# Kernel optimization log

Measured on AMD Instinct MI355X. Metric: run time of the kernel, lower is better.

## Reference

```python
import jax, jax.numpy as jnp
import numpy as np

HEADS = 20
HEAD_DIM = 64  # 1280 // 20
NUM_STYLE_TOKENS = 4
FU_SCALE = 0.5
STYLE_SCALE = 1.0
SCALE = np.float32(1.0 / np.sqrt(HEAD_DIM))


def setup_inputs() -> dict:
    key = jax.random.key(0)
    ks = jax.random.split(key, 9)
    B, S, D_MODEL, D_CROSS, T = 4, 4096, 1280, 768, 77
    sd_m = np.float32(1.0 / np.sqrt(D_MODEL))
    sd_c = np.float32(1.0 / np.sqrt(D_CROSS))
    return {
        "hidden_states": jax.random.normal(ks[0], (B, S, D_MODEL), jnp.float32),
        "encoder_hidden_states": jax.random.normal(ks[1], (B, T + NUM_STYLE_TOKENS, D_CROSS), jnp.float32),
        "Wq": jax.random.normal(ks[2], (D_MODEL, D_MODEL), jnp.float32) * sd_m,
        "Wk": jax.random.normal(ks[3], (D_CROSS, D_MODEL), jnp.float32) * sd_c,
        "Wv": jax.random.normal(ks[4], (D_CROSS, D_MODEL), jnp.float32) * sd_c,
        "Wk_ip": jax.random.normal(ks[5], (D_CROSS, D_MODEL), jnp.float32) * sd_c,
        "Wv_ip": jax.random.normal(ks[6], (D_CROSS, D_MODEL), jnp.float32) * sd_c,
        "Wo": jax.random.normal(ks[7], (D_MODEL, D_MODEL), jnp.float32) * sd_m,
        "bo": jnp.zeros((D_MODEL,), jnp.float32),
    }


def _split_heads(x, B):
    # [B, L, H*D] -> [B, H, L, D]
    return x.reshape(B, -1, HEADS, HEAD_DIM).transpose(0, 2, 1, 3)


def _attn_blend(q, k, v):
    # Manual QK^T softmax with cross-batch prob blending (fuAttn / fuIPAttn).
    probs = jax.nn.softmax(jnp.einsum('bhsd,bhtd->bhst', q, k) * SCALE, axis=-1)
    probs = probs.at[1].set(FU_SCALE * probs[1] + (1.0 - FU_SCALE) * probs[0])
    probs = probs.at[3].set(FU_SCALE * probs[3] + (1.0 - FU_SCALE) * probs[2])
    return jnp.einsum('bhst,bhtd->bhsd', probs, v)


def reference(hidden_states, encoder_hidden_states, Wq, Wk, Wv, Wk_ip, Wv_ip, Wo, bo):
    B, S, _ = hidden_states.shape
    end_pos = encoder_hidden_states.shape[1] - NUM_STYLE_TOKENS
    text = encoder_hidden_states[:, :end_pos, :]       # [B, 77, Dc]
    ip_style = encoder_hidden_states[:, end_pos:, :]   # [B, 4, Dc]

    q = _split_heads(hidden_states @ Wq, B)   # [B,H,S,D]
    k = _split_heads(text @ Wk, B)            # [B,H,77,D]
    v = _split_heads(text @ Wv, B)

    hid = _attn_blend(q, k, v).transpose(0, 2, 1, 3).reshape(B, S, -1)
    raw = hid

    ip_k = _split_heads(ip_style @ Wk_ip, B)  # [B,H,4,D]
    ip_v = _split_heads(ip_style @ Wv_ip, B)
    ip_hid = _attn_blend(q, ip_k, ip_v).transpose(0, 2, 1, 3).reshape(B, S, -1)

    hid = hid + STYLE_SCALE * ip_hid
    # batch rows 0 and 2 keep the raw (text-only) attention output
    hid = hid.at[0].set(raw[0]).at[2].set(raw[2])

    return hid @ Wo + bo
```

## Files before the change

### kernel.cpp

```cpp
#include <hip/hip_runtime.h>
#include <hip/hip_bf16.h>

typedef _Float16 half8 __attribute__((ext_vector_type(8)));
typedef _Float16 half4 __attribute__((ext_vector_type(4)));
typedef float floatx4 __attribute__((ext_vector_type(4)));

#define HEADS_ 20
#define B_    4
#define S_    4096
#define DM    1280
#define DC    768
#define TTOK  77
#define NST   4
#define EROWS 81
#define MROWS 324
#define NT_K  20

__device__ inline void gload_lds16(const void* g, void* l) {
  __builtin_amdgcn_global_load_lds((const __attribute__((address_space(1))) void*)g,
                                   (__attribute__((address_space(3))) void*)l, 16, 0, 0);
}

__global__ __launch_bounds__(256) void cast_f16(const float* __restrict__ in,
                                                _Float16* __restrict__ out, long n) {
  long i = ((long)blockIdx.x * 256 + threadIdx.x) * 8L;
  long stride = (long)gridDim.x * 256 * 8;
  for (; i < n; i += stride) {
    float4 a = *(const float4*)(in + i);
    float4 b = *(const float4*)(in + i + 4);
    half8 h;
    h[0] = (_Float16)a.x; h[1] = (_Float16)a.y; h[2] = (_Float16)a.z; h[3] = (_Float16)a.w;
    h[4] = (_Float16)b.x; h[5] = (_Float16)b.y; h[6] = (_Float16)b.z; h[7] = (_Float16)b.w;
    *(half8*)(out + i) = h;
  }
}

struct TParams { const float* in[6]; _Float16* out[6]; int R[6]; };

__global__ __launch_bounds__(256) void transpose_cast6(TParams p) {
  const int z = blockIdx.z;
  const int R = p.R[z];
  const int r0 = blockIdx.y * 32, c0 = blockIdx.x * 32;
  if (r0 >= R) return;
  const float* __restrict__ in = p.in[z];
  _Float16* __restrict__ out = p.out[z];
  __shared__ float t[32][33];
  int tx = threadIdx.x & 31, ty = threadIdx.x >> 5;
  #pragma unroll
  for (int j = 0; j < 32; j += 8)
    t[ty + j][tx] = in[(size_t)(r0 + ty + j) * DM + c0 + tx];
  __syncthreads();
  #pragma unroll
  for (int j = 0; j < 32; j += 8)
    out[(size_t)(c0 + ty + j) * R + r0 + tx] = (_Float16)t[tx][ty + j];
}

struct Ptrs4 { const _Float16* B[4]; _Float16* C[4]; };

__global__ __launch_bounds__(256) void gemm_kv(const _Float16* __restrict__ A,
                                               Ptrs4 p4, int M, int K, int N) {
  const int tid = threadIdx.x, lane = tid & 63, w = tid >> 6;
  const _Float16* Bp = p4.B[blockIdx.z];
  _Float16* Ch = p4.C[blockIdx.z];
  const int bm = blockIdx.x, bn = blockIdx.y;

  __shared__ _Float16 As[128 * 32];
  __shared__ _Float16 Bs[128 * 32];

  const int wr = (w >> 1) * 64, wc = (w & 1) * 64;
  const int arow = wr + (lane & 15), brow = wc + (lane & 15);
  const int koff = (lane >> 4) * 8;
  floatx4 acc[4][4] = {};

  const int nk = K >> 5;
  for (int kt = 0; kt < nk; ++kt) {
    #pragma unroll
    for (int c = 0; c < 2; ++c) {
      int l16 = w * 64 + lane + c * 256;
      int row = l16 >> 2, kc = (l16 & 3) << 3;
      int gr = bm * 128 + row; if (gr > M - 1) gr = M - 1;
      gload_lds16(A + (size_t)gr * K + kt * 32 + kc, &As[(w + c * 4) * 512]);
      int grb = bn * 128 + row;
      gload_lds16(Bp + (size_t)grb * K + kt * 32 + kc, &Bs[(w + c * 4) * 512]);
    }
    __syncthreads();
    half8 af[4], bf[4];
    #pragma unroll
    for (int m = 0; m < 4; m++) af[m] = *(const half8*)&As[(arow + m * 16) * 32 + koff];
    #pragma unroll
    for (int n = 0; n < 4; n++) bf[n] = *(const half8*)&Bs[(brow + n * 16) * 32 + koff];
    #pragma unroll
    for (int m = 0; m < 4; m++)
      #pragma unroll
      for (int n = 0; n < 4; n++)
        acc[m][n] = __builtin_amdgcn_mfma_f32_16x16x32_f16(af[m], bf[n], acc[m][n], 0, 0, 0);
    __syncthreads();
  }

  const int r0 = (lane >> 4) * 4, c0 = lane & 15;
  #pragma unroll
  for (int m = 0; m < 4; m++) {
    #pragma unroll
    for (int r = 0; r < 4; r++) {
      int grow = bm * 128 + wr + m * 16 + r0 + r;
      if (grow >= M) continue;
      size_t base = (size_t)grow * N + bn * 128 + wc + c0;
      #pragma unroll
      for (int n = 0; n < 4; n++) Ch[base + n * 16] = (_Float16)acc[m][n][r];
    }
  }
}

template<int OMODE>
__global__ __launch_bounds__(512, 2)
void gemm8(const _Float16* __restrict__ A,
           const _Float16* __restrict__ B,
           void* __restrict__ Cout,
           const float* __restrict__ bias) {
  __shared__ _Float16 lds[57344];
  _Float16* const A0 = lds;
  _Float16* const A1 = lds + 8192;
  _Float16* const B0 = lds + 16384;
  _Float16* const B1 = lds + 36864;

  const int tid = threadIdx.x, lane = tid & 63, w = tid >> 6;
  const int swz = (blockIdx.x & 7) * 64 + (blockIdx.x >> 3);
  const int bm = swz & 127, bn = swz >> 7;

  const int wr = w >> 2, wc = w & 3;
  const int ql = lane & 15, lg = lane >> 4, xr = ql & 7;
  const int Abase = (wr * 64 + ql) * 64;
  const int Bbase = (wc * 80 + ql) * 64;

  const int srow = tid >> 3, sslot = tid & 7;
  const int scol = ((sslot ^ (srow & 7)) << 3);
  const _Float16* const Asrc = A + (size_t)(bm * 128 + srow) * DM + scol;
  const _Float16* const Bsrc = B + (size_t)(bn * 320 + srow) * DM + scol;
  const int ldst = w * 512;

  auto stage = [&](const _Float16* src, _Float16* buf, int q, int kt) {
    gload_lds16(src + (size_t)q * 64 * DM + kt * 64, buf + q * 4096 + ldst);
  };
  auto rdA = [&](const _Float16* buf, int m, int ks) -> half8 {
    return *(const half8*)(buf + Abase + m * 1024 + (((ks * 4 + lg) ^ xr) << 3));
  };
  auto rdB = [&](const _Float16* buf, int n, int ks) -> half8 {
    return *(const half8*)(buf + Bbase + n * 1024 + (((ks * 4 + lg) ^ xr) << 3));
  };

  floatx4 acc[4][5] = {};
  half8 bF[5], bG[5];

  #pragma unroll
  for (int q = 0; q < 2; ++q) stage(Asrc, A0, q, 0);
  #pragma unroll
  for (int q = 0; q < 5; ++q) stage(Bsrc, B0, q, 0);

  auto tile_body = [&](const _Float16* Ac, const _Float16* Bc,
                       _Float16* An, _Float16* Bn, int j, bool pref) {
    if (pref) {
      #pragma unroll
      for (int q = 0; q < 2; ++q) stage(Asrc, An, q, j + 1);
      #pragma unroll
      for (int q = 0; q < 5; ++q) stage(Bsrc, Bn, q, j + 1);
      asm volatile("s_waitcnt vmcnt(7)" ::: "memory");
    } else {
      asm volatile("s_waitcnt vmcnt(0)" ::: "memory");
    }
    asm volatile("s_waitcnt lgkmcnt(0)" ::: "memory");
    __builtin_amdgcn_sched_barrier(0);
    __builtin_amdgcn_s_barrier();
    __builtin_amdgcn_sched_barrier(0);

    #pragma unroll
    for (int n = 0; n < 5; ++n) bF[n] = rdB(Bc, n, 0);
    half8 a_cur = rdA(Ac, 0, 0), a_next;
    #pragma unroll
    for (int m = 0; m < 4; ++m) {
      a_next = (m < 3) ? rdA(Ac, m + 1, 0) : rdA(Ac, 0, 1);
      if (m == 1) { bG[0] = rdB(Bc, 0, 1); bG[1] = rdB(Bc, 1, 1); }
      if (m == 2) { bG[2] = rdB(Bc, 2, 1); bG[3] = rdB(Bc, 3, 1); bG[4] = rdB(Bc, 4, 1); }
      __builtin_amdgcn_s_setprio(1);
      #pragma unroll
      for (int n = 0; n < 5; ++n)
        acc[m][n] = __builtin_amdgcn_mfma_f32_16x16x32_f16(a_cur, bF[n], acc[m][n], 0, 0, 0);
      __builtin_amdgcn_s_setprio(0);
      a_cur = a_next;
    }
    __builtin_amdgcn_s_barrier();
    #pragma unroll
    for (int m = 0; m < 4; ++m) {
      if (m < 3) a_next = rdA(Ac, m + 1, 1);
      __builtin_amdgcn_s_setprio(1);
      #pragma unroll
      for (int n = 0; n < 5; ++n)
        acc[m][n] = __builtin_amdgcn_mfma_f32_16x16x32_f16(a_cur, bG[n], acc[m][n], 0, 0, 0);
      __builtin_amdgcn_s_setprio(0);
      a_cur = a_next;
    }
  };

  for (int j = 0; j < NT_K; j += 2) {
    tile_body(A0, B0, A1, B1, j, true);
    tile_body(A1, B1, A0, B0, j + 1, j + 2 < NT_K);
  }

  const int r0 = lg * 4;
  if (OMODE == 1) {
    _Float16* Ch = (_Float16*)Cout;
    #pragma unroll
    for (int m = 0; m < 4; ++m)
      #pragma unroll
      for (int r = 0; r < 4; ++r) {
        size_t base = (size_t)(bm * 128 + wr * 64 + m * 16 + r0 + r) * DM + bn * 320 + wc * 80 + ql;
        #pragma unroll
        for (int n = 0; n < 5; ++n)
          Ch[base + n * 16] = (_Float16)(acc[m][n][r] * 0.125f);
      }
  } else {
    float* Cf = (float*)Cout;
    float bv[5];
    #pragma unroll
    for (int n = 0; n < 5; ++n) bv[n] = bias[bn * 320 + wc * 80 + n * 16 + ql];
    #pragma unroll
    for (int m = 0; m < 4; ++m)
      #pragma unroll
      for (int r = 0; r < 4; ++r) {
        size_t base = (size_t)(bm * 128 + wr * 64 + m * 16 + r0 + r) * DM + bn * 320 + wc * 80 + ql;
        #pragma unroll
        for (int n = 0; n < 5; ++n)
          Cf[base + n * 16] = acc[m][n][r] + bv[n];
      }
  }
}

template<bool ODD>
__global__ __launch_bounds__(256) void attn_kernel(const _Float16* __restrict__ Q,
                                                   const _Float16* __restrict__ kf,
                                                   const _Float16* __restrict__ vf,
                                                   const _Float16* __restrict__ ipk,
                                                   const _Float16* __restrict__ ipv,
                                                   _Float16* __restrict__ hid) {
  const int tid = threadIdx.x;
  const int h = blockIdx.y;
  const int b = blockIdx.z * 2 + (ODD ? 1 : 0);
  constexpr bool odd = ODD;
  const int hoff = h * 64;
  const int lane = tid & 63, w = tid >> 6;
  const int g = lane >> 4, ql = lane & 15;

  __shared__ _Float16 K1s[96 * 64];
  __shared__ _Float16 K2s[ODD ? 96 * 64 : 8];
  __shared__ _Float16 VTs[64 * 104];
  __shared__ char Pl[4][16 * 208];
  char* const K1c = (char*)K1s;
  char* const K2c = (char*)K2s;
  char* const VTc = (char*)VTs;
  char* const Pwc = Pl[w];

  const half8 zero8 = {};
  for (int i = tid; i < 96 * 8; i += 256) {
    int key = i >> 3, hb = i & 7;
    int dst = (key * 128 + hb * 16) ^ ((key & 7) << 4);
    half8 v = zero8;
    if (key < TTOK)
      v = *(const half8*)(kf + (size_t)(b * EROWS + key) * DM + hoff + hb * 8);
    else if (odd && key >= 80 && key < 84)
      v = *(const half8*)(ipk + (size_t)(b * EROWS + key - 3) * DM + hoff + hb * 8);
    *(half8*)(K1c + dst) = v;
    if (odd) {
      half8 v2 = zero8;
      if (key < TTOK)
        v2 = *(const half8*)(kf + (size_t)((b - 1) * EROWS + key) * DM + hoff + hb * 8);
      else if (key >= 80 && key < 84)
        v2 = *(const half8*)(ipk + (size_t)((b - 1) * EROWS + key - 3) * DM + hoff + hb * 8);
      *(half8*)(K2c + dst) = v2;
    }
  }
  for (int i = tid; i < 96 * 8; i += 256) {
    int key = i >> 3, hb = i & 7;
    half8 v = zero8;
    if (key < TTOK)
      v = *(const half8*)(vf + (size_t)(b * EROWS + key) * DM + hoff + hb * 8);
    else if (odd && key >= 80 && key < 84)
      v = *(const half8*)(ipv + (size_t)(b * EROWS + key - 3) * DM + hoff + hb * 8);
    #pragma unroll
    for (int e = 0; e < 8; ++e) VTs[(hb * 8 + e) * 104 + key] = v[e];
  }
  __syncthreads();

  for (int t = 0; t < 4; ++t) {
    const int tq0 = blockIdx.x * 256 + t * 64 + w * 16;

    const _Float16* qp = Q + (size_t)(b * S_ + tq0 + ql) * DM + hoff + g * 8;
    half8 bq0 = *(const half8*)(qp);
    half8 bq1 = *(const half8*)(qp + 32);
    half8 bq20 = zero8, bq21 = zero8;
    if (odd) {
      const _Float16* qp2 = Q + (size_t)((b - 1) * S_ + tq0 + ql) * DM + hoff + g * 8;
      bq20 = *(const half8*)(qp2);
      bq21 = *(const half8*)(qp2 + 32);
    }

    floatx4 sA[6], sB[6];
    #pragma unroll
    for (int f = 0; f < (ODD ? 6 : 5); ++f) {
      int key = f * 16 + ql;
      int sw = (key & 7) << 4;
      half8 a0 = *(const half8*)(K1c + ((key * 128 + g * 16) ^ sw));
      half8 a1 = *(const half8*)(K1c + ((key * 128 + g * 16 + 64) ^ sw));
      floatx4 z = {};
      sA[f] = __builtin_amdgcn_mfma_f32_16x16x32_f16(a0, bq0, z, 0, 0, 0);
      sA[f] = __builtin_amdgcn_mfma_f32_16x16x32_f16(a1, bq1, sA[f], 0, 0, 0);
    }
    if (odd) {
      #pragma unroll
      for (int f = 0; f < 6; ++f) {
        int key = f * 16 + ql;
        int sw = (key & 7) << 4;
        half8 a0 = *(const half8*)(K2c + ((key * 128 + g * 16) ^ sw));
        half8 a1 = *(const half8*)(K2c + ((key * 128 + g * 16 + 64) ^ sw));
        floatx4 z = {};
        sB[f] = __builtin_amdgcn_mfma_f32_16x16x32_f16(a0, bq20, z, 0, 0, 0);
        sB[f] = __builtin_amdgcn_mfma_f32_16x16x32_f16(a1, bq21, sB[f], 0, 0, 0);
      }
    }

    const int kb = g * 4;
    float mA = -1e30f;
    #pragma unroll
    for (int f = 0; f < 4; ++f)
      #pragma unroll
      for (int r = 0; r < 4; ++r) mA = fmaxf(mA, sA[f][r]);
    #pragma unroll
    for (int r = 0; r < 4; ++r) if (kb + r <= 12) mA = fmaxf(mA, sA[4][r]);
    mA = fmaxf(mA, __shfl_xor(mA, 16));
    mA = fmaxf(mA, __shfl_xor(mA, 32));
    float lA = 0.f;
    #pragma unroll
    for (int f = 0; f < 4; ++f)
      #pragma unroll
      for (int r = 0; r < 4; ++r) { float e = __expf(sA[f][r] - mA); sA[f][r] = e; lA += e; }
    #pragma unroll
    for (int r = 0; r < 4; ++r) {
      float e = (kb + r <= 12) ? __expf(sA[4][r] - mA) : 0.f;
      sA[4][r] = e; lA += e;
    }
    lA += __shfl_xor(lA, 16);
    lA += __shfl_xor(lA, 32);

    float mB = -1e30f, lB = 0.f, invB = 0.f, invIpA = 0.f, invIpB = 0.f;
    if (odd) {
      #pragma unroll
      for (int f = 0; f < 4; ++f)
        #pragma unroll
        for (int r = 0; r < 4; ++r) mB = fmaxf(mB, sB[f][r]);
      #pragma unroll
      for (int r = 0; r < 4; ++r) if (kb + r <= 12) mB = fmaxf(mB, sB[4][r]);
      mB = fmaxf(mB, __shfl_xor(mB, 16));
      mB = fmaxf(mB, __shfl_xor(mB, 32));
      #pragma unroll
      for (int f = 0; f < 4; ++f)
        #pragma unroll
        for (int r = 0; r < 4; ++r) { float e = __expf(sB[f][r] - mB); sB[f][r] = e; lB += e; }
      #pragma unroll
      for (int r = 0; r < 4; ++r) {
        float e = (kb + r <= 12) ? __expf(sB[4][r] - mB) : 0.f;
        sB[4][r] = e; lB += e;
      }
      lB += __shfl_xor(lB, 16);
      lB += __shfl_xor(lB, 32);
      invB = 0.5f / lB;

      float mia = fmaxf(fmaxf(sA[5][0], sA[5][1]), fmaxf(sA[5][2], sA[5][3]));
      float mib = fmaxf(fmaxf(sB[5][0], sB[5][1]), fmaxf(sB[5][2], sB[5][3]));
      float lia = 0.f, lib = 0.f;
      #pragma unroll
      for (int r = 0; r < 4; ++r) {
        float ea = __expf(sA[5][r] - mia); sA[5][r] = ea; lia += ea;
        float eb = __expf(sB[5][r] - mib); sB[5][r] = eb; lib += eb;
      }
      invIpA = 0.5f / lia;
      invIpB = 0.5f / lib;
    }
    const float invA = (odd ? 0.5f : 1.0f) / lA;

    asm volatile("s_waitcnt lgkmcnt(0)" ::: "memory");
    __builtin_amdgcn_sched_barrier(0);
    #pragma unroll
    for (int f = 0; f < 6; ++f) {
      #pragma unroll
      for (int r = 0; r < 4; ++r) {
        int key = f * 16 + g * 4 + r;
        float p;
        if (f < 5) p = odd ? (sA[f][r] * invA + sB[f][r] * invB) : (sA[f][r] * invA);
        else p = (odd && g == 0) ? (sA[5][r] * invIpA + sB[5][r] * invIpB) : 0.f;
        *(_Float16*)(Pwc + ql * 208 + key * 2) = (_Float16)p;
      }
    }
    asm volatile("s_waitcnt lgkmcnt(0)" ::: "memory");
    __builtin_amdgcn_sched_barrier(0);

    half8 pf[3];
    #pragma unroll
    for (int kf2 = 0; kf2 < 3; ++kf2)
      pf[kf2] = *(const half8*)(Pwc + ql * 208 + g * 16 + kf2 * 64);
    floatx4 acc_o[4] = {};
    #pragma unroll
    for (int dt = 0; dt < 4; ++dt)
      #pragma unroll
      for (int kf2 = 0; kf2 < 3; ++kf2) {
        half8 vfr = *(const half8*)(VTc + (dt * 16 + ql) * 208 + g * 16 + kf2 * 64);
        acc_o[dt] = __builtin_amdgcn_mfma_f32_16x16x32_f16(vfr, pf[kf2], acc_o[dt], 0, 0, 0);
      }

    _Float16* hr = hid + (size_t)(b * S_ + tq0 + ql) * DM + hoff;
    #pragma unroll
    for (int dt = 0; dt < 4; ++dt) {
      half4 hv;
      #pragma unroll
      for (int r = 0; r < 4; ++r) hv[r] = (_Float16)acc_o[dt][r];
      *(half4*)(hr + dt * 16 + g * 4) = hv;
    }
  }
}

extern "C" void kernel_launch(void* const* d_in, const int* in_sizes, int n_in,
                              void* d_out, int out_size, void* d_ws, size_t ws_size,
                              hipStream_t stream) {
  const float* hs   = (const float*)d_in[0];
  const float* ehs  = (const float*)d_in[1];
  const float* Wq   = (const float*)d_in[2];
  const float* Wk   = (const float*)d_in[3];
  const float* Wv   = (const float*)d_in[4];
  const float* Wkip = (const float*)d_in[5];
  const float* Wvip = (const float*)d_in[6];
  const float* Wo   = (const float*)d_in[7];
  const float* bo   = (const float*)d_in[8];
  float* out = (float*)d_out;

  char* ws = (char*)d_ws;
  size_t off = 0;
  auto alloc = [&](size_t bytes) {
    void* p = ws + off;
    off += (bytes + 255) & ~(size_t)255;
    return p;
  };
  _Float16* hs16   = (_Float16*)alloc(20971520UL * 2);
  _Float16* ehs16  = (_Float16*)alloc(248832UL * 2);
  _Float16* WqT    = (_Float16*)alloc(1638400UL * 2);
  _Float16* WoT    = (_Float16*)alloc(1638400UL * 2);
  _Float16* WkT    = (_Float16*)alloc(983040UL * 2);
  _Float16* WvT    = (_Float16*)alloc(983040UL * 2);
  _Float16* WkipT  = (_Float16*)alloc(983040UL * 2);
  _Float16* WvipT  = (_Float16*)alloc(983040UL * 2);
  _Float16* Q16    = (_Float16*)alloc(20971520UL * 2);
  _Float16* kf16   = (_Float16*)alloc(324UL * 1280 * 2);
  _Float16* vf16   = (_Float16*)alloc(324UL * 1280 * 2);
  _Float16* ipkf16 = (_Float16*)alloc(324UL * 1280 * 2);
  _Float16* ipvf16 = (_Float16*)alloc(324UL * 1280 * 2);
  _Float16* hid16 = hs16;

  cast_f16<<<2048, 256, 0, stream>>>(hs, hs16, 20971520L);
  cast_f16<<<128, 256, 0, stream>>>(ehs, ehs16, 248832L);

  TParams tp;
  tp.in[0] = Wq;   tp.out[0] = WqT;   tp.R[0] = 1280;
  tp.in[1] = Wo;   tp.out[1] = WoT;   tp.R[1] = 1280;
  tp.in[2] = Wk;   tp.out[2] = WkT;   tp.R[2] = 768;
  tp.in[3] = Wv;   tp.out[3] = WvT;   tp.R[3] = 768;
  tp.in[4] = Wkip; tp.out[4] = WkipT; tp.R[4] = 768;
  tp.in[5] = Wvip; tp.out[5] = WvipT; tp.R[5] = 768;
  transpose_cast6<<<dim3(40, 40, 6), 256, 0, stream>>>(tp);

  Ptrs4 p4;
  p4.B[0] = WkT; p4.B[1] = WvT; p4.B[2] = WkipT; p4.B[3] = WvipT;
  p4.C[0] = kf16; p4.C[1] = vf16; p4.C[2] = ipkf16; p4.C[3] = ipvf16;

  gemm_kv<<<dim3(3, 10, 4), 256, 0, stream>>>(ehs16, p4, MROWS, DC, DM);
  gemm8<1><<<512, 512, 0, stream>>>(hs16, WqT, (void*)Q16, nullptr);
  attn_kernel<false><<<dim3(16, 20, 2), 256, 0, stream>>>(Q16, kf16, vf16, ipkf16, ipvf16, hid16);
  attn_kernel<true><<<dim3(16, 20, 2), 256, 0, stream>>>(Q16, kf16, vf16, ipkf16, ipvf16, hid16);
  gemm8<2><<<512, 512, 0, stream>>>(hid16, WoT, (void*)out, bo);
}
```

Before: 223.1 us.

## Fuse fp32-to-fp16 cast of hidden states into the Q projection GEMM

The separate cast kernel that turned hidden_states into fp16 is removed. The Q GEMM now reads fp32 A tiles straight into registers during the prefetch phase, converts them, and writes them to the next LDS buffer after the MFMA work, while B still uses direct global-to-LDS loads. This removes a full read and write pass over the large activation tensor. In exchange the GEMM loads twice the A bytes, holds extra registers, and the LDS store moves onto the critical path. A barrier between the two k-substeps is also dropped in both GEMM variants.

```diff
diff --git a/kernel.cpp b/kernel.cpp
--- a/kernel.cpp
+++ b/kernel.cpp
@@ -113,7 +113,7 @@
 
 template<int OMODE>
 __global__ __launch_bounds__(512, 2)
-void gemm8(const _Float16* __restrict__ A,
+void gemm8(const void* __restrict__ Ain,
            const _Float16* __restrict__ B,
            void* __restrict__ Cout,
            const float* __restrict__ bias) {
@@ -134,12 +134,29 @@
 
   const int srow = tid >> 3, sslot = tid & 7;
   const int scol = ((sslot ^ (srow & 7)) << 3);
-  const _Float16* const Asrc = A + (size_t)(bm * 128 + srow) * DM + scol;
+  const float*    const Asrc32 = (const float*)Ain + (size_t)(bm * 128 + srow) * DM + scol;
+  const _Float16* const Asrc16 = (const _Float16*)Ain + (size_t)(bm * 128 + srow) * DM + scol;
   const _Float16* const Bsrc = B + (size_t)(bn * 320 + srow) * DM + scol;
   const int ldst = w * 512;
 
-  auto stage = [&](const _Float16* src, _Float16* buf, int q, int kt) {
-    gload_lds16(src + (size_t)q * 64 * DM + kt * 64, buf + q * 4096 + ldst);
+  auto stageA16 = [&](_Float16* buf, int q, int kt) {
+    gload_lds16(Asrc16 + (size_t)q * 64 * DM + kt * 64, buf + q * 4096 + ldst);
+  };
+  auto stageB = [&](_Float16* buf, int q, int kt) {
+    gload_lds16(Bsrc + (size_t)q * 64 * DM + kt * 64, buf + q * 4096 + ldst);
+  };
+  auto loadA32 = [&](int q, int kt, float4* dst) {
+    const float* p = Asrc32 + (size_t)q * 64 * DM + kt * 64;
+    dst[0] = *(const float4*)p;
+    dst[1] = *(const float4*)(p + 4);
+  };
+  auto writeA = [&](_Float16* buf, int q, const float4* v) {
+    half8 h;
+    h[0] = (_Float16)v[0].x; h[1] = (_Float16)v[0].y;
+    h[2] = (_Float16)v[0].z; h[3] = (_Float16)v[0].w;
+    h[4] = (_Float16)v[1].x; h[5] = (_Float16)v[1].y;
+    h[6] = (_Float16)v[1].z; h[7] = (_Float16)v[1].w;
+    *(half8*)(buf + q * 4096 + tid * 8) = h;
   };
   auto rdA = [&](const _Float16* buf, int m, int ks) -> half8 {
     return *(const half8*)(buf + Abase + m * 1024 + (((ks * 4 + lg) ^ xr) << 3));
@@ -150,20 +167,36 @@
 
   floatx4 acc[4][5] = {};
   half8 bF[5], bG[5];
-
-  #pragma unroll
-  for (int q = 0; q < 2; ++q) stage(Asrc, A0, q, 0);
-  #pragma unroll
-  for (int q = 0; q < 5; ++q) stage(Bsrc, B0, q, 0);
+  float4 aRn[4];
+
+  if constexpr (OMODE == 1) {
+    float4 aR[4];
+    loadA32(0, 0, &aR[0]); loadA32(1, 0, &aR[2]);
+    #pragma unroll
+    for (int q = 0; q < 5; ++q) stageB(B0, q, 0);
+    writeA(A0, 0, &aR[0]); writeA(A0, 1, &aR[2]);
+  } else {
+    #pragma unroll
+    for (int q = 0; q < 2; ++q) stageA16(A0, q, 0);
+    #pragma unroll
+    for (int q = 0; q < 5; ++q) stageB(B0, q, 0);
+  }
 
   auto tile_body = [&](const _Float16* Ac, const _Float16* Bc,
                        _Float16* An, _Float16* Bn, int j, bool pref) {
     if (pref) {
-      #pragma unroll
-      for (int q = 0; q < 2; ++q) stage(Asrc, An, q, j + 1);
-      #pragma unroll
-      for (int q = 0; q < 5; ++q) stage(Bsrc, Bn, q, j + 1);
-      asm volatile("s_waitcnt vmcnt(7)" ::: "memory");
+      if constexpr (OMODE == 1) {
+        loadA32(0, j + 1, &aRn[0]); loadA32(1, j + 1, &aRn[2]);
+        #pragma unroll
+        for (int q = 0; q < 5; ++q) stageB(Bn, q, j + 1);
+        asm volatile("s_waitcnt vmcnt(9)" ::: "memory");
+      } else {
+        #pragma unroll
+        for (int q = 0; q < 2; ++q) stageA16(An, q, j + 1);
+        #pragma unroll
+        for (int q = 0; q < 5; ++q) stageB(Bn, q, j + 1);
+        asm volatile("s_waitcnt vmcnt(7)" ::: "memory");
+      }
     } else {
       asm volatile("s_waitcnt vmcnt(0)" ::: "memory");
     }
@@ -187,7 +220,6 @@
       __builtin_amdgcn_s_setprio(0);
       a_cur = a_next;
     }
-    __builtin_amdgcn_s_barrier();
     #pragma unroll
     for (int m = 0; m < 4; ++m) {
       if (m < 3) a_next = rdA(Ac, m + 1, 1);
@@ -198,6 +230,9 @@
       __builtin_amdgcn_s_setprio(0);
       a_cur = a_next;
     }
+    if constexpr (OMODE == 1) {
+      if (pref) { writeA(An, 0, &aRn[0]); writeA(An, 1, &aRn[2]); }
+    }
   };
 
   for (int j = 0; j < NT_K; j += 2) {
@@ -206,7 +241,7 @@
   }
 
   const int r0 = lg * 4;
-  if (OMODE == 1) {
+  if constexpr (OMODE == 1) {
     _Float16* Ch = (_Float16*)Cout;
     #pragma unroll
     for (int m = 0; m < 4; ++m)
@@ -446,7 +481,7 @@
     off += (bytes + 255) & ~(size_t)255;
     return p;
   };
-  _Float16* hs16   = (_Float16*)alloc(20971520UL * 2);
+  _Float16* hid16  = (_Float16*)alloc(20971520UL * 2);
   _Float16* ehs16  = (_Float16*)alloc(248832UL * 2);
   _Float16* WqT    = (_Float16*)alloc(1638400UL * 2);
   _Float16* WoT    = (_Float16*)alloc(1638400UL * 2);
@@ -459,9 +494,7 @@
   _Float16* vf16   = (_Float16*)alloc(324UL * 1280 * 2);
   _Float16* ipkf16 = (_Float16*)alloc(324UL * 1280 * 2);
   _Float16* ipvf16 = (_Float16*)alloc(324UL * 1280 * 2);
-  _Float16* hid16 = hs16;
-
-  cast_f16<<<2048, 256, 0, stream>>>(hs, hs16, 20971520L);
+
   cast_f16<<<128, 256, 0, stream>>>(ehs, ehs16, 248832L);
 
   TParams tp;
@@ -478,8 +511,8 @@
   p4.C[0] = kf16; p4.C[1] = vf16; p4.C[2] = ipkf16; p4.C[3] = ipvf16;
 
   gemm_kv<<<dim3(3, 10, 4), 256, 0, stream>>>(ehs16, p4, MROWS, DC, DM);
-  gemm8<1><<<512, 512, 0, stream>>>(hs16, WqT, (void*)Q16, nullptr);
+  gemm8<1><<<512, 512, 0, stream>>>((const void*)hs, WqT, (void*)Q16, nullptr);
   attn_kernel<false><<<dim3(16, 20, 2), 256, 0, stream>>>(Q16, kf16, vf16, ipkf16, ipvf16, hid16);
   attn_kernel<true><<<dim3(16, 20, 2), 256, 0, stream>>>(Q16, kf16, vf16, ipkf16, ipvf16, hid16);
-  gemm8<2><<<512, 512, 0, stream>>>(hid16, WoT, (void*)out, bo);
-}
+  gemm8<2><<<512, 512, 0, stream>>>((const void*)hid16, WoT, (void*)out, bo);
+}
```

Result: faster. 212.4 us (-4.8%).

## Interleave global-to-LDS prefetch with MFMA phases and remap block tile order

Applied to the files above, without the earlier changes.

Restructures the GEMM main loop so the next tile's global-to-LDS loads are issued in small groups between four MFMA sub-phases, after a single barrier at the top of each tile. This replaces the old scheme that issued all prefetches up front and waited on vmcnt. The block-index mapping also changes so consecutive blocks walk the N dimension first (bn = swz & 3), which alters L2 reuse of the A and B tiles. The per-tile waits on vmcnt(0) could expose load latency, and register pressure changes because fewer B fragments are held at once.

```diff
diff --git a/kernel.cpp b/kernel.cpp
--- a/kernel.cpp
+++ b/kernel.cpp
@@ -125,7 +125,7 @@
 
   const int tid = threadIdx.x, lane = tid & 63, w = tid >> 6;
   const int swz = (blockIdx.x & 7) * 64 + (blockIdx.x >> 3);
-  const int bm = swz & 127, bn = swz >> 7;
+  const int bm = swz >> 2, bn = swz & 3;
 
   const int wr = w >> 2, wc = w & 3;
   const int ql = lane & 15, lg = lane >> 4, xr = ql & 7;
@@ -138,8 +138,11 @@
   const _Float16* const Bsrc = B + (size_t)(bn * 320 + srow) * DM + scol;
   const int ldst = w * 512;
 
-  auto stage = [&](const _Float16* src, _Float16* buf, int q, int kt) {
-    gload_lds16(src + (size_t)q * 64 * DM + kt * 64, buf + q * 4096 + ldst);
+  auto stageA = [&](_Float16* buf, int q, int kt) {
+    gload_lds16(Asrc + (size_t)q * 64 * DM + kt * 64, buf + q * 4096 + ldst);
+  };
+  auto stageB = [&](_Float16* buf, int q, int kt) {
+    gload_lds16(Bsrc + (size_t)q * 64 * DM + kt * 64, buf + q * 4096 + ldst);
   };
   auto rdA = [&](const _Float16* buf, int m, int ks) -> half8 {
     return *(const half8*)(buf + Abase + m * 1024 + (((ks * 4 + lg) ^ xr) << 3));
@@ -149,55 +152,67 @@
   };
 
   floatx4 acc[4][5] = {};
-  half8 bF[5], bG[5];
+  half8 bF[5], aF[2];
 
   #pragma unroll
-  for (int q = 0; q < 2; ++q) stage(Asrc, A0, q, 0);
+  for (int q = 0; q < 2; ++q) stageA(A0, q, 0);
   #pragma unroll
-  for (int q = 0; q < 5; ++q) stage(Bsrc, B0, q, 0);
+  for (int q = 0; q < 5; ++q) stageB(B0, q, 0);
 
   auto tile_body = [&](const _Float16* Ac, const _Float16* Bc,
                        _Float16* An, _Float16* Bn, int j, bool pref) {
-    if (pref) {
-      #pragma unroll
-      for (int q = 0; q < 2; ++q) stage(Asrc, An, q, j + 1);
-      #pragma unroll
-      for (int q = 0; q < 5; ++q) stage(Bsrc, Bn, q, j + 1);
-      asm volatile("s_waitcnt vmcnt(7)" ::: "memory");
-    } else {
-      asm volatile("s_waitcnt vmcnt(0)" ::: "memory");
-    }
+    asm volatile("s_waitcnt vmcnt(0)" ::: "memory");
+    __builtin_amdgcn_sched_barrier(0);
+    __builtin_amdgcn_s_barrier();
+    __builtin_amdgcn_sched_barrier(0);
+    if (pref) { stageA(An, 0, j + 1); stageA(An, 1, j + 1); }
+    #pragma unroll
+    for (int n = 0; n < 5; ++n) bF[n] = rdB(Bc, n, 0);
+    aF[0] = rdA(Ac, 0, 0); aF[1] = rdA(Ac, 1, 0);
     asm volatile("s_waitcnt lgkmcnt(0)" ::: "memory");
     __builtin_amdgcn_sched_barrier(0);
-    __builtin_amdgcn_s_barrier();
-    __builtin_amdgcn_sched_barrier(0);
-
-    #pragma unroll
-    for (int n = 0; n < 5; ++n) bF[n] = rdB(Bc, n, 0);
-    half8 a_cur = rdA(Ac, 0, 0), a_next;
-    #pragma unroll
-    for (int m = 0; m < 4; ++m) {
-      a_next = (m < 3) ? rdA(Ac, m + 1, 0) : rdA(Ac, 0, 1);
-      if (m == 1) { bG[0] = rdB(Bc, 0, 1); bG[1] = rdB(Bc, 1, 1); }
-      if (m == 2) { bG[2] = rdB(Bc, 2, 1); bG[3] = rdB(Bc, 3, 1); bG[4] = rdB(Bc, 4, 1); }
-      __builtin_amdgcn_s_setprio(1);
+    __builtin_amdgcn_s_setprio(1);
+    #pragma unroll
+    for (int m = 0; m < 2; ++m)
       #pragma unroll
       for (int n = 0; n < 5; ++n)
-        acc[m][n] = __builtin_amdgcn_mfma_f32_16x16x32_f16(a_cur, bF[n], acc[m][n], 0, 0, 0);
-      __builtin_amdgcn_s_setprio(0);
-      a_cur = a_next;
-    }
-    __builtin_amdgcn_s_barrier();
-    #pragma unroll
-    for (int m = 0; m < 4; ++m) {
-      if (m < 3) a_next = rdA(Ac, m + 1, 1);
-      __builtin_amdgcn_s_setprio(1);
+        acc[m][n] = __builtin_amdgcn_mfma_f32_16x16x32_f16(aF[m], bF[n], acc[m][n], 0, 0, 0);
+    __builtin_amdgcn_s_setprio(0);
+    if (pref) { stageB(Bn, 0, j + 1); stageB(Bn, 1, j + 1); }
+    aF[0] = rdA(Ac, 2, 0); aF[1] = rdA(Ac, 3, 0);
+    asm volatile("s_waitcnt lgkmcnt(0)" ::: "memory");
+    __builtin_amdgcn_sched_barrier(0);
+    __builtin_amdgcn_s_setprio(1);
+    #pragma unroll
+    for (int m = 0; m < 2; ++m)
       #pragma unroll
       for (int n = 0; n < 5; ++n)
-        acc[m][n] = __builtin_amdgcn_mfma_f32_16x16x32_f16(a_cur, bG[n], acc[m][n], 0, 0, 0);
-      __builtin_amdgcn_s_setprio(0);
-      a_cur = a_next;
-    }
+        acc[2 + m][n] = __builtin_amdgcn_mfma_f32_16x16x32_f16(aF[m], bF[n], acc[2 + m][n], 0, 0, 0);
+    __builtin_amdgcn_s_setprio(0);
+    if (pref) { stageB(Bn, 2, j + 1); stageB(Bn, 3, j + 1); }
+    #pragma unroll
+    for (int n = 0; n < 5; ++n) bF[n] = rdB(Bc, n, 1);
+    aF[0] = rdA(Ac, 0, 1); aF[1] = rdA(Ac, 1, 1);
+    asm volatile("s_waitcnt lgkmcnt(0)" ::: "memory");
+    __builtin_amdgcn_sched_barrier(0);
+    __builtin_amdgcn_s_setprio(1);
+    #pragma unroll
+    for (int m = 0; m < 2; ++m)
+      #pragma unroll
+      for (int n = 0; n < 5; ++n)
+        acc[m][n] = __builtin_amdgcn_mfma_f32_16x16x32_f16(aF[m], bF[n], acc[m][n], 0, 0, 0);
+    __builtin_amdgcn_s_setprio(0);
+    if (pref) { stageB(Bn, 4, j + 1); }
+    aF[0] = rdA(Ac, 2, 1); aF[1] = rdA(Ac, 3, 1);
+    asm volatile("s_waitcnt lgkmcnt(0)" ::: "memory");
+    __builtin_amdgcn_sched_barrier(0);
+    __builtin_amdgcn_s_setprio(1);
+    #pragma unroll
+    for (int m = 0; m < 2; ++m)
+      #pragma unroll
+      for (int n = 0; n < 5; ++n)
+        acc[2 + m][n] = __builtin_amdgcn_mfma_f32_16x16x32_f16(aF[m], bF[n], acc[2 + m][n], 0, 0, 0);
+    __builtin_amdgcn_s_setprio(0);
   };
 
   for (int j = 0; j < NT_K; j += 2) {
@@ -206,7 +221,7 @@
   }
 
   const int r0 = lg * 4;
-  if (OMODE == 1) {
+  if constexpr (OMODE == 1) {
     _Float16* Ch = (_Float16*)Cout;
     #pragma unroll
     for (int m = 0; m < 4; ++m)
```

After: 215.5 us. 3.4% less time.
